# Kernel optimization log

Measured on AMD Instinct MI355X. Metric: run time of the kernel, lower is better.

## Reference

```python
import jax, jax.numpy as jnp
import numpy as np

N_NODES = 20000
N_EDGES = 320000
N_GRAPHS = 512
N_FEAT = 29
DIMS = [N_FEAT, 1024, 512, 256, 512, 1024]
EPS = 1e-5


def setup_inputs() -> dict:
    key = jax.random.key(0)
    ks = jax.random.split(key, 32)
    inp = {}
    inp["x"] = jax.random.normal(ks[0], (N_NODES, N_FEAT), dtype=jnp.float32)
    inp["edge_index"] = jax.random.randint(ks[1], (2, N_EDGES), 0, N_NODES, dtype=jnp.int64)
    inp["batch"] = jnp.sort(jax.random.randint(ks[2], (N_NODES,), 0, N_GRAPHS, dtype=jnp.int64))
    # 5 GCNConv layers: weight [in, out] + bias, plus BN gamma/beta
    for i in range(5):
        din, dout = DIMS[i], DIMS[i + 1]
        inp[f"W{i+1}"] = jax.random.normal(ks[3 + i], (din, dout), dtype=jnp.float32) * (1.0 / np.sqrt(din))
        inp[f"b{i+1}"] = jnp.zeros((dout,), dtype=jnp.float32)
        inp[f"g{i+1}"] = jnp.ones((dout,), dtype=jnp.float32)
        inp[f"be{i+1}"] = jnp.zeros((dout,), dtype=jnp.float32)
    # attention gate Linear(1024, 1)
    inp["Wg"] = jax.random.normal(ks[10], (1024, 1), dtype=jnp.float32) * 0.03
    inp["bg"] = jnp.zeros((1,), dtype=jnp.float32)
    # MLP head
    inp["Wf2"] = jax.random.normal(ks[11], (1024, 128), dtype=jnp.float32) * 0.03
    inp["bf2"] = jnp.zeros((128,), dtype=jnp.float32)
    inp["Wf3"] = jax.random.normal(ks[12], (128, 16), dtype=jnp.float32) * 0.25
    inp["bf3"] = jnp.zeros((16,), dtype=jnp.float32)
    inp["Wf4"] = jax.random.normal(ks[13], (16, 1), dtype=jnp.float32) * 0.25
    inp["bf4"] = jnp.zeros((1,), dtype=jnp.float32)
    return inp


def _gcn_conv(x, row, col, W, b):
    # PyG GCNConv: linear transform, then D^{-1/2}(A+I)D^{-1/2} aggregation, then bias.
    n = x.shape[0]
    xw = x @ W  # [N, dout]
    deg = jax.ops.segment_sum(jnp.ones_like(col, dtype=xw.dtype), col, num_segments=n)
    dinv = jnp.where(deg > 0, jax.lax.rsqrt(deg), 0.0)
    norm = dinv[row] * dinv[col]  # [E+N]
    out = jax.ops.segment_sum(xw[row] * norm[:, None], col, num_segments=n)
    return out + b


def _bn_train(x, gamma, beta):
    m = jnp.mean(x, axis=0)
    v = jnp.var(x, axis=0)  # biased, matches torch training normalization
    return gamma * (x - m) * jax.lax.rsqrt(v + EPS) + beta


def _global_attention(x, batch, Wg, bg, n_graphs):
    gate = (x @ Wg + bg)[:, 0]  # [N]
    gmax = jax.ops.segment_max(gate, batch, num_segments=n_graphs)
    e = jnp.exp(gate - gmax[batch])
    s = jax.ops.segment_sum(e, batch, num_segments=n_graphs)
    alpha = e / s[batch]
    return jax.ops.segment_sum(alpha[:, None] * x, batch, num_segments=n_graphs)


def reference(x, edge_index, batch,
              W1, b1, g1, be1, W2, b2, g2, be2, W3, b3, g3, be3,
              W4, b4, g4, be4, W5, b5, g5, be5,
              Wg, bg, Wf2, bf2, Wf3, bf3, Wf4, bf4):
    n = x.shape[0]
    sl = jnp.arange(n, dtype=edge_index.dtype)
    row = jnp.concatenate([edge_index[0], sl])  # with self-loops
    col = jnp.concatenate([edge_index[1], sl])
    h = x
    params = [(W1, b1, g1, be1), (W2, b2, g2, be2), (W3, b3, g3, be3),
              (W4, b4, g4, be4), (W5, b5, g5, be5)]
    for (W, b, g, be) in params:
        h = jax.nn.relu(_gcn_conv(h, row, col, W, b))
        h = _bn_train(h, g, be)
    p = _global_attention(h, batch, Wg, bg, N_GRAPHS)  # [G, 1024]
    p = jax.nn.relu(p @ Wf2 + bf2)
    p = jax.nn.relu(p @ Wf3 + bf3)
    return p @ Wf4 + bf4  # [G, 1]
```

## Files before the change

kernel.cpp:

```cpp
#include <hip/hip_runtime.h>

#define EPS_BN 1e-5f

constexpr int NN   = 20000;
constexpr int NE   = 320000;
constexpr int NTOT = NE + NN;
constexpr int NG   = 512;
constexpr int MPAD = 20480;

typedef _Float16 half8  __attribute__((ext_vector_type(8)));
typedef _Float16 half2v __attribute__((ext_vector_type(2)));
typedef float floatx4   __attribute__((ext_vector_type(4)));

__device__ __forceinline__ void gload_lds16(const void* g, void* l) {
  __builtin_amdgcn_global_load_lds(
      (const __attribute__((address_space(1))) void*)g,
      (__attribute__((address_space(3))) void*)l, 16, 0, 0);
}

__global__ void k_deg(const int* __restrict__ col, int* __restrict__ deg,
                      const int* __restrict__ batch, int* __restrict__ gcnt) {
  int e = blockIdx.x * blockDim.x + threadIdx.x;
  if (e >= NTOT) return;
  int c = (e < NE) ? col[e] : (e - NE);
  atomicAdd(&deg[c], 1);
  if (e < NN) atomicAdd(&gcnt[batch[e]], 1);
}

__global__ __launch_bounds__(1024) void k_scan(const int* __restrict__ counts, int n,
                                               int* __restrict__ out_ptr,
                                               int* __restrict__ cursor,
                                               float* __restrict__ dinvv) {
  __shared__ int ssum[1024];
  int tid = threadIdx.x;
  int per = (n + 1023) / 1024;
  int beg = tid * per;
  int end = min(beg + per, n);
  int s = 0;
  for (int i = beg; i < end; ++i) {
    s += counts[i];
    if (dinvv) dinvv[i] = rsqrtf((float)counts[i]);
  }
  ssum[tid] = s;
  __syncthreads();
  for (int off = 1; off < 1024; off <<= 1) {
    int v = ssum[tid];
    int add = (tid >= off) ? ssum[tid - off] : 0;
    __syncthreads();
    ssum[tid] = v + add;
    __syncthreads();
  }
  int excl = (tid == 0) ? 0 : ssum[tid - 1];
  for (int i = beg; i < end; ++i) {
    out_ptr[i] = excl;
    cursor[i]  = excl;
    excl += counts[i];
  }
  if (tid == 1023) out_ptr[n] = ssum[1023];
}

__global__ void k_fill(const int* __restrict__ row, const int* __restrict__ col,
                       const float* __restrict__ dinv, int* __restrict__ cursor,
                       int2* __restrict__ csw, float* __restrict__ rsum) {
  int e = blockIdx.x * blockDim.x + threadIdx.x;
  if (e >= NTOT) return;
  int r, c;
  if (e < NE) { r = row[e]; c = col[e]; } else { r = c = e - NE; }
  float wv = dinv[r] * dinv[c];
  int pos = atomicAdd(&cursor[c], 1);
  int2 m; m.x = r; m.y = __builtin_bit_cast(int, wv);
  csw[pos] = m;
  atomicAdd(&rsum[c], wv);
}

__global__ void k_wconv3(const float* __restrict__ W0, const float* __restrict__ W3,
                         const float* __restrict__ W4,
                         _Float16* __restrict__ T0, _Float16* __restrict__ T3,
                         _Float16* __restrict__ T4) {
  int idx = blockIdx.x * blockDim.x + threadIdx.x;
  if (idx < 32768) {
    int n = idx >> 5, k = idx & 31;
    T0[idx] = (_Float16)((k < 29) ? W0[(size_t)k * 1024 + n] : 0.f);
  } else if (idx < 32768 + 131072) {
    int j = idx - 32768;
    int n = j >> 8, k = j & 255;
    T3[j] = (_Float16)W3[(size_t)k * 512 + n];
  } else if (idx < 32768 + 131072 + 524288) {
    int j = idx - 163840;
    int n = j >> 9, k = j & 511;
    T4[j] = (_Float16)W4[(size_t)k * 1024 + n];
  }
}

__global__ __launch_bounds__(256) void k_wfold(const float* __restrict__ W, int K, int N,
                                               const float* __restrict__ sums,
                                               const float* __restrict__ gamma,
                                               const float* __restrict__ beta,
                                               _Float16* __restrict__ T,
                                               float* __restrict__ c) {
  __shared__ float red[256];
  int n = blockIdx.x, tid = threadIdx.x;
  const float inv_n = 1.f / NN;
  float csum = 0.f;
  for (int k = tid; k < K; k += 256) {
    float mean = sums[k] * inv_n;
    float var  = sums[K + k] * inv_n - mean * mean;
    float sc   = gamma[k] * rsqrtf(var + EPS_BN);
    float sh   = beta[k] - mean * sc;
    float wv   = W[(size_t)k * N + n];
    T[(size_t)n * K + k] = (_Float16)(sc * wv);
    csum += sh * wv;
  }
  red[tid] = csum;
  __syncthreads();
  for (int o = 128; o > 0; o >>= 1) {
    if (tid < o) red[tid] += red[tid + o];
    __syncthreads();
  }
  if (tid == 0) c[n] = red[0];
}

#define AGG_T  128
#define AGG_CH 128
__global__ __launch_bounds__(AGG_T) void k_agg29(
    const float* __restrict__ X,
    const int* __restrict__ indptr, const int2* __restrict__ csw,
    _Float16* __restrict__ Y) {
  __shared__ int   s_src[AGG_CH];
  __shared__ float s_w[AGG_CH];
  int node = blockIdx.x;
  int tid  = threadIdx.x;
  int beg = indptr[node], end = indptr[node + 1];
  float acc = 0.f;
  for (int e0 = beg; e0 < end; e0 += AGG_CH) {
    int c = min(AGG_CH, end - e0);
    if (tid < c) {
      int2 m = csw[e0 + tid];
      s_src[tid] = m.x;
      s_w[tid]   = __builtin_bit_cast(float, m.y);
    }
    __syncthreads();
    for (int j = 0; j < c; ++j) {
      if (tid < 29) acc += s_w[j] * X[(size_t)s_src[j] * 29 + tid];
    }
    __syncthreads();
  }
  if (tid < 32) Y[(size_t)node * 32 + tid] = (tid < 29) ? (_Float16)acc : (_Float16)0.f;
}

template<int VEC, int MODE>
__global__ __launch_bounds__(256) void k_aggv(
    const _Float16* __restrict__ X, _Float16* __restrict__ Y,
    const int* __restrict__ indptr, const int2* __restrict__ csw,
    const float* __restrict__ rowsum,
    const float* __restrict__ p0, const float* __restrict__ p1,
    const float* __restrict__ p2)
{
  constexpr int F = 64 * VEC;
  int wave = threadIdx.x >> 6;
  int lane = threadIdx.x & 63;
  int node = blockIdx.x * 4 + wave;
  int beg = indptr[node], end = indptr[node + 1];
  float acc[VEC];
  #pragma unroll
  for (int i = 0; i < VEC; ++i) acc[i] = 0.f;
  const unsigned* Xl = (const unsigned*)X + lane * (VEC / 2);

  auto body = [&](int e) {
    int2 m = csw[e];
    float we = __builtin_bit_cast(float, m.y);
    const unsigned* xr = Xl + (size_t)m.x * (F / 2);
    unsigned uu[VEC / 2];
    if constexpr (VEC == 8) {
      uint4 d = *(const uint4*)xr;
      uu[0] = d.x; uu[1] = d.y; uu[2] = d.z; uu[3] = d.w;
    } else {
      uint2 d = *(const uint2*)xr;
      uu[0] = d.x; uu[1] = d.y;
    }
    #pragma unroll
    for (int i = 0; i < VEC / 2; ++i) {
      half2v h = __builtin_bit_cast(half2v, uu[i]);
      acc[2 * i]     = fmaf(we, (float)h[0], acc[2 * i]);
      acc[2 * i + 1] = fmaf(we, (float)h[1], acc[2 * i + 1]);
    }
  };
  int e = beg;
  for (; e + 4 <= end; e += 4) { body(e); body(e + 1); body(e + 2); body(e + 3); }
  for (; e < end; ++e) body(e);

  float s_n = rowsum[node];
  size_t ob = (size_t)node * F + lane * VEC;
  _Float16 outv[VEC];
  #pragma unroll
  for (int i = 0; i < VEC; ++i) {
    int f = lane * VEC + i;
    float v;
    if constexpr (MODE == 0) {
      v = fmaxf(acc[i] + s_n * p0[f] + p1[f], 0.f);
    } else {
      const float inv_n = 1.f / NN;
      float mean = p0[f] * inv_n;
      float var  = p0[F + f] * inv_n - mean * mean;
      float sc   = p1[f] * rsqrtf(var + EPS_BN);
      float sh   = p2[f] - mean * sc;
      v = sc * acc[i] + s_n * sh;
    }
    outv[i] = (_Float16)v;
  }
  if constexpr (VEC == 8) *(uint4*)(Y + ob) = *(const uint4*)outv;
  else                    *(uint2*)(Y + ob) = *(const uint2*)outv;
}

template<int BK>
__global__ __launch_bounds__(256) void k_gemm16(
    const _Float16* __restrict__ A, const _Float16* __restrict__ B,
    const float* __restrict__ bias,
    _Float16* __restrict__ Ch,
    float* __restrict__ stats,
    int N, int K, int do_relu, int nbx)
{
  __shared__ __align__(16) union UU {
    struct { _Float16 a[128 * BK]; _Float16 b[128 * BK]; } ab;
    _Float16 c[128 * 136];
  } u;
  __shared__ float sred[256];

  const int tid  = threadIdx.x;
  const int wave = tid >> 6;
  const int lane = tid & 63;

  int lin = blockIdx.x;
  int xcd = lin & 7, seq = lin >> 3;
  int bx = seq % nbx, grp = seq / nbx;
  int by = xcd + 8 * grp;
  const int row0 = by * 128;
  const int col0 = bx * 128;

  const int q  = lane >> 4;
  const int mm = lane & 15;
  const int wm = wave >> 1;
  const int wn = wave & 1;

  sred[tid] = 0.f;

  constexpr int NREP = (BK == 32) ? 2 : 4;
  constexpr int RPW  = (BK == 32) ? 16 : 8;
  const _Float16* pA[NREP];
  const _Float16* pB[NREP];
  _Float16* dstA[NREP];
  _Float16* dstB[NREP];
  {
    int rl = (BK == 32) ? (lane >> 2) : (lane >> 3);
    int cp = (BK == 32) ? (lane & 3) : (lane & 7);
    #pragma unroll
    for (int rep = 0; rep < NREP; ++rep) {
      int trow = wave * 32 + rep * RPW;
      int s = (BK == 32) ? ((lane >> 3) & 3) : ((rep & 1) * 4 + (rl >> 1));
      int csrc = cp ^ s;
      pA[rep] = A + (size_t)(row0 + trow + rl) * K + csrc * 8;
      pB[rep] = B + (size_t)(col0 + trow + rl) * K + csrc * 8;
      dstA[rep] = u.ab.a + trow * BK;
      dstB[rep] = u.ab.b + trow * BK;
    }
  }

  const int sR = (BK == 32) ? ((mm >> 1) & 3) : (mm >> 1);
  int rdA[4], rdB[4];
  #pragma unroll
  for (int i = 0; i < 4; ++i) {
    rdA[i] = (wm * 64 + i * 16 + mm) * BK;
    rdB[i] = (wn * 64 + i * 16 + mm) * BK;
  }

  floatx4 acc[4][4];
  #pragma unroll
  for (int i = 0; i < 4; ++i)
    #pragma unroll
    for (int j = 0; j < 4; ++j) acc[i][j] = floatx4{0.f, 0.f, 0.f, 0.f};

  for (int k0 = 0; k0 < K; k0 += BK) {
    #pragma unroll
    for (int rep = 0; rep < NREP; ++rep) {
      gload_lds16(pA[rep], dstA[rep]);
      gload_lds16(pB[rep], dstB[rep]);
      pA[rep] += BK; pB[rep] += BK;
    }
    __syncthreads();

    #pragma unroll
    for (int kk = 0; kk < BK / 32; ++kk) {
      int pos = ((q + 4 * kk) ^ sR) * 8;
      half8 av[4];
      #pragma unroll
      for (int i = 0; i < 4; ++i) av[i] = *(const half8*)&u.ab.a[rdA[i] + pos];
      #pragma unroll
      for (int j = 0; j < 4; ++j) {
        half8 bv = *(const half8*)&u.ab.b[rdB[j] + pos];
        #pragma unroll
        for (int i = 0; i < 4; ++i)
          acc[i][j] = __builtin_amdgcn_mfma_f32_16x16x32_f16(av[i], bv, acc[i][j], 0, 0, 0);
      }
    }
    __syncthreads();
  }

  float sloc[4]  = {0.f, 0.f, 0.f, 0.f};
  float s2loc[4] = {0.f, 0.f, 0.f, 0.f};
  #pragma unroll
  for (int j = 0; j < 4; ++j) {
    int cl = wn * 64 + j * 16 + mm;
    float bv = bias ? bias[col0 + cl] : 0.f;
    #pragma unroll
    for (int i = 0; i < 4; ++i) {
      #pragma unroll
      for (int r = 0; r < 4; ++r) {
        int rl = wm * 64 + i * 16 + q * 4 + r;
        float v = acc[i][j][r] + bv;
        if (do_relu) v = fmaxf(v, 0.f);
        u.c[rl * 136 + cl] = (_Float16)v;
        if (row0 + rl < NN) { sloc[j] += v; s2loc[j] += v * v; }
      }
    }
  }

  if (stats) {
    #pragma unroll
    for (int j = 0; j < 4; ++j) {
      float a = sloc[j], b2 = s2loc[j];
      a  += __shfl_xor(a, 16, 64);  a  += __shfl_xor(a, 32, 64);
      b2 += __shfl_xor(b2, 16, 64); b2 += __shfl_xor(b2, 32, 64);
      if (q == 0) {
        int cl = wn * 64 + j * 16 + mm;
        atomicAdd(&sred[cl], a);
        atomicAdd(&sred[128 + cl], b2);
      }
    }
  }
  __syncthreads();

  #pragma unroll
  for (int pass = 0; pass < 8; ++pass) {
    int cidx = tid + pass * 256;
    int r = cidx >> 4, kc = cidx & 15;
    int rr = row0 + r;
    if (rr < NN) {
      uint4 d = *(const uint4*)&u.c[r * 136 + kc * 8];
      *(uint4*)&Ch[(size_t)rr * N + col0 + kc * 8] = d;
    }
  }

  if (stats && tid < 128) {
    atomicAdd(&stats[col0 + tid], sred[tid]);
    atomicAdd(&stats[N + col0 + tid], sred[128 + tid]);
  }
}

__global__ __launch_bounds__(256) void k_stats16(const _Float16* __restrict__ X, int F,
                                                 float* __restrict__ sums) {
  int tid = threadIdx.x;
  int npf = F >> 8;
  float s[2] = {0.f, 0.f}, s2[2] = {0.f, 0.f};
  for (int r = blockIdx.x; r < NN; r += gridDim.x) {
    #pragma unroll
    for (int i = 0; i < 2; ++i) {
      if (i < npf) {
        float v = (float)X[(size_t)r * F + tid + i * 256];
        s[i] += v; s2[i] += v * v;
      }
    }
  }
  #pragma unroll
  for (int i = 0; i < 2; ++i) {
    if (i < npf) {
      atomicAdd(&sums[tid + i * 256], s[i]);
      atomicAdd(&sums[F + tid + i * 256], s2[i]);
    }
  }
}

__global__ __launch_bounds__(1024) void k_prep(const float* __restrict__ sums,
                                               const float* __restrict__ g5,
                                               const float* __restrict__ be5,
                                               const float* __restrict__ Wg,
                                               const float* __restrict__ bg,
                                               float* __restrict__ sc, float* __restrict__ sh,
                                               float* __restrict__ scWg, float* __restrict__ gconst) {
  __shared__ float red[1024];
  int f = threadIdx.x;
  const float inv_n = 1.f / NN;
  float mean = sums[f] * inv_n;
  float var  = sums[1024 + f] * inv_n - mean * mean;
  float s = g5[f] * rsqrtf(var + EPS_BN);
  float h = be5[f] - mean * s;
  sc[f] = s; sh[f] = h;
  float wgf = Wg[f];
  scWg[f] = s * wgf;
  red[f] = h * wgf;
  __syncthreads();
  for (int o = 512; o > 0; o >>= 1) {
    if (f < o) red[f] += red[f + o];
    __syncthreads();
  }
  if (f == 0) gconst[0] = red[0] + bg[0];
}

__global__ __launch_bounds__(256) void k_gate_aff(const _Float16* __restrict__ X,
                                                  const float* __restrict__ scWg,
                                                  const float* __restrict__ gconst,
                                                  float* __restrict__ gate) {
  __shared__ float red[256];
  int n = blockIdx.x, tid = threadIdx.x;
  int f = tid * 4;
  uint2 u = *(const uint2*)(X + (size_t)n * 1024 + f);
  half2v h0 = __builtin_bit_cast(half2v, u.x);
  half2v h1 = __builtin_bit_cast(half2v, u.y);
  float s = (float)h0[0] * scWg[f] + (float)h0[1] * scWg[f + 1]
          + (float)h1[0] * scWg[f + 2] + (float)h1[1] * scWg[f + 3];
  red[tid] = s;
  __syncthreads();
  for (int o = 128; o > 0; o >>= 1) {
    if (tid < o) red[tid] += red[tid + o];
    __syncthreads();
  }
  if (tid == 0) gate[n] = red[0] + gconst[0];
}

__global__ __launch_bounds__(64) void k_segred(const float* __restrict__ gate,
                                               const int* __restrict__ goff,
                                               float* __restrict__ gmax,
                                               float* __restrict__ gsum) {
  int g = blockIdx.x, tid = threadIdx.x;
  int beg = goff[g], end = goff[g + 1];
  float m = -3.4e38f;
  for (int n = beg + tid; n < end; n += 64) m = fmaxf(m, gate[n]);
  for (int o = 32; o > 0; o >>= 1) m = fmaxf(m, __shfl_down(m, o, 64));
  m = __shfl(m, 0, 64);
  float s = 0.f;
  for (int n = beg + tid; n < end; n += 64) s += expf(gate[n] - m);
  for (int o = 32; o > 0; o >>= 1) s += __shfl_down(s, o, 64);
  if (tid == 0) { gmax[g] = m; gsum[g] = s; }
}

__global__ __launch_bounds__(256) void k_pool_aff(const _Float16* __restrict__ X,
                                                  const float* __restrict__ gate,
                                                  const int* __restrict__ goff,
                                                  const float* __restrict__ gmax,
                                                  const float* __restrict__ gsum,
                                                  const float* __restrict__ sc,
                                                  const float* __restrict__ sh,
                                                  float* __restrict__ pooled) {
  int g = blockIdx.x, tid = threadIdx.x;
  int beg = goff[g], end = goff[g + 1];
  int f = tid * 4;
  float acc[4] = {0.f, 0.f, 0.f, 0.f};
  bool nonempty = end > beg;
  if (nonempty) {
    float m = gmax[g], inv = 1.f / gsum[g];
    for (int n = beg; n < end; ++n) {
      float a = expf(gate[n] - m) * inv;
      uint2 u = *(const uint2*)(X + (size_t)n * 1024 + f);
      half2v h0 = __builtin_bit_cast(half2v, u.x);
      half2v h1 = __builtin_bit_cast(half2v, u.y);
      acc[0] += a * (float)h0[0];
      acc[1] += a * (float)h0[1];
      acc[2] += a * (float)h1[0];
      acc[3] += a * (float)h1[1];
    }
  }
  #pragma unroll
  for (int i = 0; i < 4; ++i) {
    int ff = f + i;
    float v = nonempty ? (acc[i] * sc[ff] + sh[ff]) : 0.f;
    pooled[(size_t)g * 1024 + ff] = v;
  }
}

__global__ __launch_bounds__(128) void k_head(const float* __restrict__ pooled,
                                              const float* __restrict__ Wf2, const float* __restrict__ bf2,
                                              const float* __restrict__ Wf3, const float* __restrict__ bf3,
                                              const float* __restrict__ Wf4, const float* __restrict__ bf4,
                                              float* __restrict__ out) {
  __shared__ float sp[1024];
  __shared__ float sp2[128];
  __shared__ float sp3[16];
  int g = blockIdx.x, tid = threadIdx.x;
  #pragma unroll
  for (int i = 0; i < 8; ++i) sp[tid + i * 128] = pooled[(size_t)g * 1024 + tid + i * 128];
  __syncthreads();
  float s = bf2[tid];
  for (int k = 0; k < 1024; ++k) s += sp[k] * Wf2[k * 128 + tid];
  sp2[tid] = fmaxf(s, 0.f);
  __syncthreads();
  if (tid < 16) {
    float t = bf3[tid];
    for (int k = 0; k < 128; ++k) t += sp2[k] * Wf3[k * 16 + tid];
    sp3[tid] = fmaxf(t, 0.f);
  }
  __syncthreads();
  if (tid == 0) {
    float t = bf4[0];
    for (int k = 0; k < 16; ++k) t += sp3[k] * Wf4[k];
    out[g] = t;
  }
}

extern "C" void kernel_launch(void* const* d_in, const int* in_sizes, int n_in,
                              void* d_out, int out_size, void* d_ws, size_t ws_size,
                              hipStream_t stream) {
  const float* x     = (const float*)d_in[0];
  const int*   ei    = (const int*)d_in[1];
  const int*   batch = (const int*)d_in[2];
  const float* W[5]; const float* b[5]; const float* g[5]; const float* be[5];
  for (int l = 0; l < 5; ++l) {
    W[l]  = (const float*)d_in[3 + 4 * l];
    b[l]  = (const float*)d_in[4 + 4 * l];
    g[l]  = (const float*)d_in[5 + 4 * l];
    be[l] = (const float*)d_in[6 + 4 * l];
  }
  const float* Wg  = (const float*)d_in[23];
  const float* bg  = (const float*)d_in[24];
  const float* Wf2 = (const float*)d_in[25];
  const float* bf2 = (const float*)d_in[26];
  const float* Wf3 = (const float*)d_in[27];
  const float* bf3 = (const float*)d_in[28];
  const float* Wf4 = (const float*)d_in[29];
  const float* bf4 = (const float*)d_in[30];
  float* out = (float*)d_out;

  const int* row = ei;
  const int* col = ei + NE;

  char* base = (char*)d_ws;
  size_t off = 0;
  auto alloc = [&](size_t bytes) -> char* {
    char* p = base + off;
    off = (off + bytes + 255) & ~(size_t)255;
    return p;
  };
  _Float16*  AH  = (_Float16*)alloc((size_t)MPAD * 1024 * 2);
  _Float16*  ASM = (_Float16*)alloc((size_t)MPAD * 32 * 2);
  _Float16*  BF  = (_Float16*)alloc((size_t)NN * 512 * 2);
  _Float16*  BF2 = (_Float16*)alloc((size_t)NN * 512 * 2);
  _Float16*  H5  = (_Float16*)alloc((size_t)NN * 1024 * 2);
  const int wtsz[5] = {1024 * 32, 512 * 1024, 256 * 512, 512 * 256, 1024 * 512};
  _Float16* WT[5];
  for (int l = 0; l < 5; ++l) WT[l] = (_Float16*)alloc((size_t)wtsz[l] * 2);
  float* c2  = (float*)alloc(512 * 4);
  float* c3  = (float*)alloc(256 * 4);
  float* dinv    = (float*)alloc(NN * 4);
  int*   indptr  = (int*)alloc((NN + 1) * 4);
  int*   cursor  = (int*)alloc(NN * 4);
  int2*  csw     = (int2*)alloc((size_t)NTOT * 8);
  int*   goff    = (int*)alloc((NG + 1) * 4);
  int*   gcur    = (int*)alloc(NG * 4);
  float* gate    = (float*)alloc(NN * 4);
  float* gmax    = (float*)alloc(NG * 4);
  float* gsum    = (float*)alloc(NG * 4);
  float* pooled  = (float*)alloc((size_t)NG * 1024 * 4);
  float* scv5 = (float*)alloc(1024 * 4);
  float* shv5 = (float*)alloc(1024 * 4);
  float* scWg = (float*)alloc(1024 * 4);
  float* gconst = (float*)alloc(4);
  size_t znf = 6656 + NN + NG + NN;
  float* zbase = (float*)alloc(znf * 4);
  float* bns  = zbase;
  int*   deg  = (int*)(zbase + 6656);
  int*   gcnt = (int*)(zbase + 6656 + NN);
  float* rsum = zbase + 6656 + NN + NG;
  float* bns1 = bns;
  float* bns2 = bns + 2048;
  float* bns3 = bns + 3072;
  float* bns4 = bns + 3584;
  float* bns5 = bns + 4608;

  hipMemsetAsync(zbase, 0, znf * 4, stream);
  k_deg<<<(NTOT + 255) / 256, 256, 0, stream>>>(col, deg, batch, gcnt);
  k_scan<<<1, 1024, 0, stream>>>(deg, NN, indptr, cursor, dinv);
  k_fill<<<(NTOT + 255) / 256, 256, 0, stream>>>(row, col, dinv, cursor, csw, rsum);
  k_scan<<<1, 1024, 0, stream>>>(gcnt, NG, goff, gcur, nullptr);
  k_wconv3<<<2688, 256, 0, stream>>>(W[0], W[3], W[4], WT[0], WT[3], WT[4]);

  auto gemm = [&](const _Float16* Aop, int wl, const float* bias,
                  _Float16* Ch, float* stats, int Nn, int Kk, int relu) {
    int nbx = Nn / 128;
    if (Kk == 32)
      k_gemm16<32><<<nbx * 160, 256, 0, stream>>>(Aop, WT[wl], bias, Ch, stats, Nn, Kk, relu, nbx);
    else
      k_gemm16<64><<<nbx * 160, 256, 0, stream>>>(Aop, WT[wl], bias, Ch, stats, Nn, Kk, relu, nbx);
  };

  k_agg29<<<NN, AGG_T, 0, stream>>>(x, indptr, csw, ASM);
  gemm(ASM, 0, b[0], AH, bns1, 1024, 32, 1);

  k_wfold<<<512, 256, 0, stream>>>(W[1], 1024, 512, bns1, g[0], be[0], WT[1], c2);
  gemm(AH, 1, nullptr, BF, nullptr, 512, 1024, 0);
  k_aggv<8, 0><<<NN / 4, 256, 0, stream>>>(BF, AH, indptr, csw, rsum, c2, b[1], nullptr);
  k_stats16<<<512, 256, 0, stream>>>(AH, 512, bns2);

  k_wfold<<<256, 256, 0, stream>>>(W[2], 512, 256, bns2, g[1], be[1], WT[2], c3);
  gemm(AH, 2, nullptr, BF2, nullptr, 256, 512, 0);
  k_aggv<4, 0><<<NN / 4, 256, 0, stream>>>(BF2, BF, indptr, csw, rsum, c3, b[2], nullptr);
  k_stats16<<<512, 256, 0, stream>>>(BF, 256, bns3);

  k_aggv<4, 1><<<NN / 4, 256, 0, stream>>>(BF, AH, indptr, csw, rsum, bns3, g[2], be[2]);
  gemm(AH, 3, b[3], BF2, bns4, 512, 256, 1);

  k_aggv<8, 1><<<NN / 4, 256, 0, stream>>>(BF2, AH, indptr, csw, rsum, bns4, g[3], be[3]);
  gemm(AH, 4, b[4], H5, bns5, 1024, 512, 1);

  k_prep<<<1, 1024, 0, stream>>>(bns5, g[4], be[4], Wg, bg, scv5, shv5, scWg, gconst);
  k_gate_aff<<<NN, 256, 0, stream>>>(H5, scWg, gconst, gate);
  k_segred<<<NG, 64, 0, stream>>>(gate, goff, gmax, gsum);
  k_pool_aff<<<NG, 256, 0, stream>>>(H5, gate, goff, gmax, gsum, scv5, shv5, pooled);

  k_head<<<NG, 128, 0, stream>>>(pooled, Wf2, bf2, Wf3, bf3, Wf4, bf4, out);
}
```

Baseline: 693.0 us.

## Replace LDS-staged GEMM with direct global MFMA loads and parallelize prefix scans

The GEMM no longer stages A/B tiles in LDS through global_load_lds. Each lane now loads its MFMA fragments straight from global memory, with K made a template constant and the loop unrolled by two. The single-block 1024-thread scans are replaced by a three-kernel multi-block wave-shuffle scan, and the aggregation edge loop is unrolled by eight. Dropping LDS staging removes the barriers, but the two waves sharing a tile now each fetch the A/B data from memory or cache, which raises global traffic.

```diff
diff --git a/kernel.cpp b/kernel.cpp
--- a/kernel.cpp
+++ b/kernel.cpp
@@ -7,16 +7,11 @@
 constexpr int NTOT = NE + NN;
 constexpr int NG   = 512;
 constexpr int MPAD = 20480;
+constexpr int NBLK = 79;
 
 typedef _Float16 half8  __attribute__((ext_vector_type(8)));
 typedef _Float16 half2v __attribute__((ext_vector_type(2)));
 typedef float floatx4   __attribute__((ext_vector_type(4)));
-
-__device__ __forceinline__ void gload_lds16(const void* g, void* l) {
-  __builtin_amdgcn_global_load_lds(
-      (const __attribute__((address_space(1))) void*)g,
-      (__attribute__((address_space(3))) void*)l, 16, 0, 0);
-}
 
 __global__ void k_deg(const int* __restrict__ col, int* __restrict__ deg,
                       const int* __restrict__ batch, int* __restrict__ gcnt) {
@@ -27,36 +22,69 @@
   if (e < NN) atomicAdd(&gcnt[batch[e]], 1);
 }
 
-__global__ __launch_bounds__(1024) void k_scan(const int* __restrict__ counts, int n,
-                                               int* __restrict__ out_ptr,
-                                               int* __restrict__ cursor,
-                                               float* __restrict__ dinvv) {
-  __shared__ int ssum[1024];
-  int tid = threadIdx.x;
-  int per = (n + 1023) / 1024;
-  int beg = tid * per;
-  int end = min(beg + per, n);
-  int s = 0;
-  for (int i = beg; i < end; ++i) {
-    s += counts[i];
-    if (dinvv) dinvv[i] = rsqrtf((float)counts[i]);
-  }
-  ssum[tid] = s;
-  __syncthreads();
-  for (int off = 1; off < 1024; off <<= 1) {
-    int v = ssum[tid];
-    int add = (tid >= off) ? ssum[tid - off] : 0;
-    __syncthreads();
-    ssum[tid] = v + add;
-    __syncthreads();
-  }
-  int excl = (tid == 0) ? 0 : ssum[tid - 1];
-  for (int i = beg; i < end; ++i) {
-    out_ptr[i] = excl;
-    cursor[i]  = excl;
-    excl += counts[i];
-  }
-  if (tid == 1023) out_ptr[n] = ssum[1023];
+__global__ __launch_bounds__(256) void k_pre1(const int* __restrict__ deg,
+                                              float* __restrict__ dinvv,
+                                              int* __restrict__ psum) {
+  __shared__ int ws[4];
+  int t = threadIdx.x, lane = t & 63, wv = t >> 6;
+  int idx = blockIdx.x * 256 + t;
+  int d = (idx < NN) ? deg[idx] : 0;
+  if (idx < NN) dinvv[idx] = rsqrtf((float)d);
+  int s = d;
+  for (int o = 1; o < 64; o <<= 1) { int u = __shfl_up(s, o, 64); if (lane >= o) s += u; }
+  if (lane == 63) ws[wv] = s;
+  __syncthreads();
+  if (t == 0) psum[blockIdx.x] = ws[0] + ws[1] + ws[2] + ws[3];
+}
+
+__global__ __launch_bounds__(256) void k_pre2(const int* __restrict__ psum,
+                                              int* __restrict__ pbase,
+                                              const int* __restrict__ gcnt,
+                                              int* __restrict__ goff) {
+  __shared__ int ws[8];
+  int t = threadIdx.x, lane = t & 63, wv = t >> 6;
+  int v = (t < NBLK) ? psum[t] : 0;
+  int inc = v;
+  for (int o = 1; o < 64; o <<= 1) { int u = __shfl_up(inc, o, 64); if (lane >= o) inc += u; }
+  if (lane == 63) ws[wv] = inc;
+  __syncthreads();
+  int base = 0;
+  for (int w = 0; w < wv; ++w) base += ws[w];
+  int excl = base + inc - v;
+  if (t < NBLK) pbase[t] = excl;
+  if (t == NBLK - 1) pbase[NBLK] = excl + v;
+  __syncthreads();
+  int a0 = gcnt[2 * t], a1 = gcnt[2 * t + 1];
+  int p = a0 + a1;
+  int incp = p;
+  for (int o = 1; o < 64; o <<= 1) { int u = __shfl_up(incp, o, 64); if (lane >= o) incp += u; }
+  if (lane == 63) ws[4 + wv] = incp;
+  __syncthreads();
+  int gb = 0;
+  for (int w = 0; w < wv; ++w) gb += ws[4 + w];
+  int exclp = gb + incp - p;
+  goff[2 * t]     = exclp;
+  goff[2 * t + 1] = exclp + a0;
+  if (t == 255) goff[NG] = exclp + p;
+}
+
+__global__ __launch_bounds__(256) void k_pre3(const int* __restrict__ deg,
+                                              const int* __restrict__ pbase,
+                                              int* __restrict__ indptr,
+                                              int* __restrict__ cursor) {
+  __shared__ int ws[4];
+  int t = threadIdx.x, lane = t & 63, wv = t >> 6;
+  int idx = blockIdx.x * 256 + t;
+  int d = (idx < NN) ? deg[idx] : 0;
+  int inc = d;
+  for (int o = 1; o < 64; o <<= 1) { int u = __shfl_up(inc, o, 64); if (lane >= o) inc += u; }
+  if (lane == 63) ws[wv] = inc;
+  __syncthreads();
+  int base = pbase[blockIdx.x];
+  for (int w = 0; w < wv; ++w) base += ws[w];
+  int excl = base + inc - d;
+  if (idx < NN) { indptr[idx] = excl; cursor[idx] = excl; }
+  if (idx == NN - 1) indptr[NN] = excl + d;
 }
 
 __global__ void k_fill(const int* __restrict__ row, const int* __restrict__ col,
@@ -186,7 +214,10 @@
     }
   };
   int e = beg;
-  for (; e + 4 <= end; e += 4) { body(e); body(e + 1); body(e + 2); body(e + 3); }
+  for (; e + 8 <= end; e += 8) {
+    body(e); body(e + 1); body(e + 2); body(e + 3);
+    body(e + 4); body(e + 5); body(e + 6); body(e + 7);
+  }
   for (; e < end; ++e) body(e);
 
   float s_n = rowsum[node];
@@ -212,18 +243,15 @@
   else                    *(uint2*)(Y + ob) = *(const uint2*)outv;
 }
 
-template<int BK>
-__global__ __launch_bounds__(256) void k_gemm16(
+template<int K>
+__global__ __launch_bounds__(256) void k_gemmg(
     const _Float16* __restrict__ A, const _Float16* __restrict__ B,
     const float* __restrict__ bias,
     _Float16* __restrict__ Ch,
     float* __restrict__ stats,
-    int N, int K, int do_relu, int nbx)
+    int N, int do_relu, int nbx)
 {
-  __shared__ __align__(16) union UU {
-    struct { _Float16 a[128 * BK]; _Float16 b[128 * BK]; } ab;
-    _Float16 c[128 * 136];
-  } u;
+  __shared__ __align__(16) _Float16 cs[128 * 136];
   __shared__ float sred[256];
 
   const int tid  = threadIdx.x;
@@ -244,34 +272,14 @@
 
   sred[tid] = 0.f;
 
-  constexpr int NREP = (BK == 32) ? 2 : 4;
-  constexpr int RPW  = (BK == 32) ? 16 : 8;
-  const _Float16* pA[NREP];
-  const _Float16* pB[NREP];
-  _Float16* dstA[NREP];
-  _Float16* dstB[NREP];
-  {
-    int rl = (BK == 32) ? (lane >> 2) : (lane >> 3);
-    int cp = (BK == 32) ? (lane & 3) : (lane & 7);
-    #pragma unroll
-    for (int rep = 0; rep < NREP; ++rep) {
-      int trow = wave * 32 + rep * RPW;
-      int s = (BK == 32) ? ((lane >> 3) & 3) : ((rep & 1) * 4 + (rl >> 1));
-      int csrc = cp ^ s;
-      pA[rep] = A + (size_t)(row0 + trow + rl) * K + csrc * 8;
-      pB[rep] = B + (size_t)(col0 + trow + rl) * K + csrc * 8;
-      dstA[rep] = u.ab.a + trow * BK;
-      dstB[rep] = u.ab.b + trow * BK;
-    }
-  }
-
-  const int sR = (BK == 32) ? ((mm >> 1) & 3) : (mm >> 1);
-  int rdA[4], rdB[4];
-  #pragma unroll
-  for (int i = 0; i < 4; ++i) {
-    rdA[i] = (wm * 64 + i * 16 + mm) * BK;
-    rdB[i] = (wn * 64 + i * 16 + mm) * BK;
-  }
+  const _Float16* pa[4];
+  const _Float16* pb[4];
+  #pragma unroll
+  for (int i = 0; i < 4; ++i)
+    pa[i] = A + (size_t)(row0 + wm * 64 + i * 16 + mm) * K + q * 8;
+  #pragma unroll
+  for (int j = 0; j < 4; ++j)
+    pb[j] = B + (size_t)(col0 + wn * 64 + j * 16 + mm) * K + q * 8;
 
   floatx4 acc[4][4];
   #pragma unroll
@@ -279,30 +287,18 @@
     #pragma unroll
     for (int j = 0; j < 4; ++j) acc[i][j] = floatx4{0.f, 0.f, 0.f, 0.f};
 
-  for (int k0 = 0; k0 < K; k0 += BK) {
-    #pragma unroll
-    for (int rep = 0; rep < NREP; ++rep) {
-      gload_lds16(pA[rep], dstA[rep]);
-      gload_lds16(pB[rep], dstB[rep]);
-      pA[rep] += BK; pB[rep] += BK;
-    }
-    __syncthreads();
-
-    #pragma unroll
-    for (int kk = 0; kk < BK / 32; ++kk) {
-      int pos = ((q + 4 * kk) ^ sR) * 8;
-      half8 av[4];
+  #pragma unroll 2
+  for (int k0 = 0; k0 < K; k0 += 32) {
+    half8 av[4], bv[4];
+    #pragma unroll
+    for (int i = 0; i < 4; ++i) { av[i] = *(const half8*)pa[i]; pa[i] += 32; }
+    #pragma unroll
+    for (int j = 0; j < 4; ++j) { bv[j] = *(const half8*)pb[j]; pb[j] += 32; }
+    #pragma unroll
+    for (int j = 0; j < 4; ++j)
       #pragma unroll
-      for (int i = 0; i < 4; ++i) av[i] = *(const half8*)&u.ab.a[rdA[i] + pos];
-      #pragma unroll
-      for (int j = 0; j < 4; ++j) {
-        half8 bv = *(const half8*)&u.ab.b[rdB[j] + pos];
-        #pragma unroll
-        for (int i = 0; i < 4; ++i)
-          acc[i][j] = __builtin_amdgcn_mfma_f32_16x16x32_f16(av[i], bv, acc[i][j], 0, 0, 0);
-      }
-    }
-    __syncthreads();
+      for (int i = 0; i < 4; ++i)
+        acc[i][j] = __builtin_amdgcn_mfma_f32_16x16x32_f16(av[i], bv[j], acc[i][j], 0, 0, 0);
   }
 
   float sloc[4]  = {0.f, 0.f, 0.f, 0.f};
@@ -318,7 +314,7 @@
         int rl = wm * 64 + i * 16 + q * 4 + r;
         float v = acc[i][j][r] + bv;
         if (do_relu) v = fmaxf(v, 0.f);
-        u.c[rl * 136 + cl] = (_Float16)v;
+        cs[rl * 136 + cl] = (_Float16)v;
         if (row0 + rl < NN) { sloc[j] += v; s2loc[j] += v * v; }
       }
     }
@@ -345,7 +341,7 @@
     int r = cidx >> 4, kc = cidx & 15;
     int rr = row0 + r;
     if (rr < NN) {
-      uint4 d = *(const uint4*)&u.c[r * 136 + kc * 8];
+      uint4 d = *(const uint4*)&cs[r * 136 + kc * 8];
       *(uint4*)&Ch[(size_t)rr * N + col0 + kc * 8] = d;
     }
   }
@@ -552,8 +548,9 @@
   int*   indptr  = (int*)alloc((NN + 1) * 4);
   int*   cursor  = (int*)alloc(NN * 4);
   int2*  csw     = (int2*)alloc((size_t)NTOT * 8);
+  int*   psum    = (int*)alloc((NBLK + 1) * 4);
+  int*   pbase   = (int*)alloc((NBLK + 1) * 4);
   int*   goff    = (int*)alloc((NG + 1) * 4);
-  int*   gcur    = (int*)alloc(NG * 4);
   float* gate    = (float*)alloc(NN * 4);
   float* gmax    = (float*)alloc(NG * 4);
   float* gsum    = (float*)alloc(NG * 4);
@@ -576,18 +573,20 @@
 
   hipMemsetAsync(zbase, 0, znf * 4, stream);
   k_deg<<<(NTOT + 255) / 256, 256, 0, stream>>>(col, deg, batch, gcnt);
-  k_scan<<<1, 1024, 0, stream>>>(deg, NN, indptr, cursor, dinv);
+  k_pre1<<<NBLK, 256, 0, stream>>>(deg, dinv, psum);
+  k_pre2<<<1, 256, 0, stream>>>(psum, pbase, gcnt, goff);
+  k_pre3<<<NBLK, 256, 0, stream>>>(deg, pbase, indptr, cursor);
   k_fill<<<(NTOT + 255) / 256, 256, 0, stream>>>(row, col, dinv, cursor, csw, rsum);
-  k_scan<<<1, 1024, 0, stream>>>(gcnt, NG, goff, gcur, nullptr);
   k_wconv3<<<2688, 256, 0, stream>>>(W[0], W[3], W[4], WT[0], WT[3], WT[4]);
 
   auto gemm = [&](const _Float16* Aop, int wl, const float* bias,
                   _Float16* Ch, float* stats, int Nn, int Kk, int relu) {
     int nbx = Nn / 128;
-    if (Kk == 32)
-      k_gemm16<32><<<nbx * 160, 256, 0, stream>>>(Aop, WT[wl], bias, Ch, stats, Nn, Kk, relu, nbx);
-    else
-      k_gemm16<64><<<nbx * 160, 256, 0, stream>>>(Aop, WT[wl], bias, Ch, stats, Nn, Kk, relu, nbx);
+    dim3 grid(nbx * 160);
+    if      (Kk == 32)   k_gemmg<32>  <<<grid, 256, 0, stream>>>(Aop, WT[wl], bias, Ch, stats, Nn, relu, nbx);
+    else if (Kk == 256)  k_gemmg<256> <<<grid, 256, 0, stream>>>(Aop, WT[wl], bias, Ch, stats, Nn, relu, nbx);
+    else if (Kk == 512)  k_gemmg<512> <<<grid, 256, 0, stream>>>(Aop, WT[wl], bias, Ch, stats, Nn, relu, nbx);
+    else                 k_gemmg<1024><<<grid, 256, 0, stream>>>(Aop, WT[wl], bias, Ch, stats, Nn, relu, nbx);
   };
 
   k_agg29<<<NN, AGG_T, 0, stream>>>(x, indptr, csw, ASM);
```

Measured after the change: 753.8 us. 8.8% more time.
